# Kernel optimization log

Measured on AMD Instinct MI355X. Metric: run time of the kernel, lower is better.

## Reference

```python
import jax, jax.numpy as jnp
import numpy as np

DIM = 256
NH = 8
HD = DIM // NH
SCALE = HD ** -0.5


def setup_inputs() -> dict:
    key = jax.random.key(0)
    ks = jax.random.split(key, 11)
    Bn, Mh, Mw, C = 2048, 8, 8, DIM
    x = jax.random.normal(ks[0], (Bn, Mh, Mw, C), dtype=jnp.float32)
    y = jax.random.normal(ks[1], (Bn, Mh, Mw, C), dtype=jnp.float32)
    z = jax.random.normal(ks[2], (Bn, Mh, Mw, C), dtype=jnp.float32)
    s = 0.02
    q_w = jax.random.normal(ks[3], (C, C), dtype=jnp.float32) * s
    q_b = jnp.zeros((C,), dtype=jnp.float32)
    k_w = jax.random.normal(ks[4], (C, C), dtype=jnp.float32) * s
    k_b = jnp.zeros((C,), dtype=jnp.float32)
    v_w = jax.random.normal(ks[5], (C, C), dtype=jnp.float32) * s
    v_b = jnp.zeros((C,), dtype=jnp.float32)
    proj_w = jax.random.normal(ks[6], (C, C), dtype=jnp.float32) * s
    proj_b = jnp.zeros((C,), dtype=jnp.float32)
    return {"x": x, "y": y, "z": z, "q_w": q_w, "q_b": q_b, "k_w": k_w,
            "k_b": k_b, "v_w": v_w, "v_b": v_b, "proj_w": proj_w, "proj_b": proj_b}


def softmax_plus_one(a):
    m = jnp.max(a, axis=-1, keepdims=True)
    e = jnp.exp(a - m)
    return e / (jnp.sum(e, axis=-1, keepdims=True) + 1.0)


def reference(x, y, z, q_w, q_b, k_w, k_b, v_w, v_b, proj_w, proj_b):
    Bn, Mh, Mw, C = x.shape
    L = Mh * Mw
    xf = x.reshape(Bn, L, C)
    yf = y.reshape(Bn, L, C)
    # z is rearranged but unused in the original forward

    def heads(t, w, b):
        # torch Linear: t @ w.T + b, then split heads -> (Bn, Nh, L, HD)
        p = t @ w.T + b
        return p.reshape(Bn, L, NH, HD).transpose(0, 2, 1, 3)

    q1 = heads(yf, q_w, q_b) * SCALE
    k1 = heads(xf, k_w, k_b)
    v1 = heads(xf, v_w, v_b)

    attn = jnp.einsum('bnqd,bnkd->bnqk', q1, k1)  # (Bn, Nh, L, L)
    attn = softmax_plus_one(attn)
    y1 = jnp.einsum('bnqk,bnkd->bnqd', attn, v1)  # (Bn, Nh, L, HD)
    y1 = y1.transpose(0, 2, 1, 3).reshape(Bn, Mh, Mw, C)

    out = y + y1
    out = out @ proj_w.T + proj_b
    return out
```

## Files before the change

### kernel.cpp

```cpp
#include <hip/hip_runtime.h>

typedef __bf16 bf16x8 __attribute__((ext_vector_type(8)));
typedef __bf16 bf16x4 __attribute__((ext_vector_type(4)));
typedef short  s16x4  __attribute__((ext_vector_type(4)));
typedef float  f32x4  __attribute__((ext_vector_type(4)));
typedef unsigned int u32x4 __attribute__((ext_vector_type(4)));
typedef unsigned int u32x2 __attribute__((ext_vector_type(2)));
typedef unsigned int u32;
typedef unsigned short u16;

#define DEVI static __device__ __forceinline__

static constexpr float KSCALE = 0.17677669529663687f;

DEVI u32 pk2(float a, float b){
  u16 ha = __builtin_bit_cast(u16, (__bf16)a);
  u16 hb = __builtin_bit_cast(u16, (__bf16)b);
  return (u32)ha | ((u32)hb << 16);
}
DEVI float bfl(u32 bits16){
  union { u32 i; float f; } v; v.i = bits16 << 16; return v.f;
}
DEVI u32x2 pkfrag(f32x4 v){ u32x2 o; o[0]=pk2(v[0],v[1]); o[1]=pk2(v[2],v[3]); return o; }
DEVI bf16x8 ld16(const void* p){ return __builtin_bit_cast(bf16x8, *(const u32x4*)p); }
DEVI f32x4 mfma16(bf16x8 a, bf16x8 b, f32x4 c){
  return __builtin_amdgcn_mfma_f32_16x16x32_bf16(a, b, c, 0, 0, 0);
}
DEVI f32x4 mfma1616(u32x2 a, u32x2 b, f32x4 c){
#if __has_builtin(__builtin_amdgcn_mfma_f32_16x16x16_bf16)
  return __builtin_amdgcn_mfma_f32_16x16x16_bf16(
      __builtin_bit_cast(bf16x4, a), __builtin_bit_cast(bf16x4, b), c, 0, 0, 0);
#elif __has_builtin(__builtin_amdgcn_mfma_f32_16x16x16bf16_1k)
  return __builtin_amdgcn_mfma_f32_16x16x16bf16_1k(
      __builtin_bit_cast(s16x4, a), __builtin_bit_cast(s16x4, b), c, 0, 0, 0);
#else
  asm("v_mfma_f32_16x16x16_bf16 %0, %1, %2, %0" : "+v"(c) : "v"(a), "v"(b));
  return c;
#endif
}

template<bool BW>
DEVI bf16x8 loadw(const u16* wbp, const float* wfp){
  if constexpr (BW){
    return ld16(wbp);
  } else {
    f32x4 a = *(const f32x4*)wfp;
    f32x4 b = *(const f32x4*)(wfp + 4);
    u32x4 pc; pc[0]=pk2(a[0],a[1]); pc[1]=pk2(a[2],a[3]); pc[2]=pk2(b[0],b[1]); pc[3]=pk2(b[2],b[3]);
    return __builtin_bit_cast(bf16x8, pc);
  }
}

__global__ void prep_w(const float* __restrict__ qw, const float* __restrict__ kw,
                       const float* __restrict__ vw, const float* __restrict__ pw,
                       u16* __restrict__ dst){
  int blk = blockIdx.x;
  int l   = threadIdx.x;
  int M = blk >> 7, R = (blk >> 3) & 15, kk = blk & 7;
  const float* W = (M==0) ? qw : (M==1) ? kw : (M==2) ? vw : pw;
  const float* src = W + (R*16 + (l&15))*256 + kk*32 + (l>>4)*8;
  f32x4 a  = *(const f32x4*)src;
  f32x4 b2 = *(const f32x4*)(src + 4);
  u32x4 pc; pc[0]=pk2(a[0],a[1]); pc[1]=pk2(a[2],a[3]); pc[2]=pk2(b2[0],b2[1]); pc[3]=pk2(b2[2],b2[3]);
  *(u32x4*)(dst + (size_t)blk*512 + l*8) = pc;
}

DEVI const u16* wfrag(const u16* wb, int M, int R, int kk, int l){
  return wb + ((((M<<4) + R)<<3) + kk)*512 + l*8;
}

template<bool BW>
__global__ __launch_bounds__(256, 2)
void fused_ca(const float* __restrict__ x, const float* __restrict__ y,
              const u16* __restrict__ wb,
              const float* __restrict__ qwf, const float* __restrict__ kwf,
              const float* __restrict__ vwf, const float* __restrict__ pwf,
              const float* __restrict__ qb, const float* __restrict__ kb,
              const float* __restrict__ vb, const float* __restrict__ pb,
              float* __restrict__ out)
{
  extern __shared__ char smem[];
  const int b  = blockIdx.x;
  const int t  = threadIdx.x;
  const int w  = t >> 6;
  const int l  = t & 63;
  const int lo = l & 15;
  const int g  = l >> 4;
  const u32 swr = (u32)(lo & 7) << 4;

  char* r1 = smem;
  char* Xs = smem + 32768;

  const float* yb = y + (size_t)b * 16384;
  const float* xb = x + (size_t)b * 16384;

  #pragma unroll
  for (int j = 0; j < 16; ++j){
    int idx = t + 256*j;
    int row = idx >> 6;
    int c0  = (idx & 63) * 4;
    f32x4 v = *(const f32x4*)(yb + row*256 + c0);
    u32x2 o; o[0] = pk2(v[0], v[1]); o[1] = pk2(v[2], v[3]);
    *(u32x2*)(r1 + row*512 + ((u32)(c0*2) ^ ((u32)(row&7) << 4))) = o;
  }
  f32x4 xr[8];
  #pragma unroll
  for (int j = 0; j < 8; ++j){
    int idx = t + 256*j;
    xr[j] = *(const f32x4*)(xb + (idx>>6)*256 + (idx & 63)*4);
  }
  __syncthreads();

  u32x2 aqpk[2][8];
  #pragma unroll
  for (int hl = 0; hl < 2; ++hl){
    const int cb = w*64 + hl*32;
    const int Rb = w*4 + hl*2;
    f32x4 aq[2][4] = {};
    #pragma unroll
    for (int kk = 0; kk < 8; ++kk){
      bf16x8 A[2], Bf[4];
      #pragma unroll
      for (int m = 0; m < 2; ++m){
        int off = (cb + 16*m + lo)*256 + kk*32 + 8*g;
        A[m] = loadw<BW>(wfrag(wb, 0, Rb + m, kk, l), qwf + off);
      }
      #pragma unroll
      for (int n = 0; n < 4; ++n)
        Bf[n] = ld16(r1 + (16*n+lo)*512 + ((u32)(kk*64 + 16*g) ^ swr));
      #pragma unroll
      for (int m = 0; m < 2; ++m)
        #pragma unroll
        for (int n = 0; n < 4; ++n)
          aq[m][n] = mfma16(A[m], Bf[n], aq[m][n]);
    }
    #pragma unroll
    for (int m = 0; m < 2; ++m){
      f32x4 bias = *(const f32x4*)(qb + cb + 16*m + 4*g);
      #pragma unroll
      for (int n = 0; n < 4; ++n){
        f32x4 v; 
        #pragma unroll
        for (int r = 0; r < 4; ++r) v[r] = (aq[m][n][r] + bias[r]) * KSCALE;
        aqpk[hl][m*4+n] = pkfrag(v);
      }
    }
    if (hl == 0){
      #pragma unroll
      for (int j = 0; j < 8; ++j){
        int idx = t + 256*j;
        int row = idx >> 6;
        int c0  = (idx & 63) * 4;
        u32x2 o; o[0] = pk2(xr[j][0], xr[j][1]); o[1] = pk2(xr[j][2], xr[j][3]);
        *(u32x2*)(Xs + row*512 + ((u32)(c0*2) ^ ((u32)(row&7) << 4))) = o;
      }
      #pragma unroll
      for (int j = 0; j < 8; ++j){
        int idx = t + 256*(j+8);
        xr[j] = *(const f32x4*)(xb + (idx>>6)*256 + (idx & 63)*4);
      }
    }
  }
  #pragma unroll
  for (int j = 0; j < 8; ++j){
    int idx = t + 256*(j+8);
    int row = idx >> 6;
    int c0  = (idx & 63) * 4;
    u32x2 o; o[0] = pk2(xr[j][0], xr[j][1]); o[1] = pk2(xr[j][2], xr[j][3]);
    *(u32x2*)(Xs + row*512 + ((u32)(c0*2) ^ ((u32)(row&7) << 4))) = o;
  }
  __syncthreads();

  #pragma unroll
  for (int hl = 0; hl < 2; ++hl){
    const int cb = w*64 + hl*32;
    const int Rb = w*4 + hl*2;

    f32x4 ak[2][4] = {};
    f32x4 av[4][2] = {};
    #pragma unroll
    for (int kk = 0; kk < 8; ++kk){
      bf16x8 WA[2], WB2[2], XF[4];
      #pragma unroll
      for (int m = 0; m < 2; ++m){
        int off = (cb + 16*m + lo)*256 + kk*32 + 8*g;
        WA[m] = loadw<BW>(wfrag(wb, 1, Rb + m, kk, l), kwf + off);
      }
      #pragma unroll
      for (int n = 0; n < 2; ++n){
        int off = (cb + 16*n + lo)*256 + kk*32 + 8*g;
        WB2[n] = loadw<BW>(wfrag(wb, 2, Rb + n, kk, l), vwf + off);
      }
      #pragma unroll
      for (int f = 0; f < 4; ++f)
        XF[f] = ld16(Xs + (16*f+lo)*512 + ((u32)(kk*64 + 16*g) ^ swr));
      #pragma unroll
      for (int f = 0; f < 4; ++f){
        #pragma unroll
        for (int m = 0; m < 2; ++m)
          ak[m][f] = mfma16(WA[m], XF[f], ak[m][f]);
        #pragma unroll
        for (int n = 0; n < 2; ++n)
          av[f][n] = mfma16(XF[f], WB2[n], av[f][n]);
      }
    }
    u32x2 akpk[8], avpk[8];
    #pragma unroll
    for (int m = 0; m < 2; ++m){
      f32x4 bias = *(const f32x4*)(kb + cb + 16*m + 4*g);
      #pragma unroll
      for (int f = 0; f < 4; ++f){
        f32x4 v;
        #pragma unroll
        for (int r = 0; r < 4; ++r) v[r] = ak[m][f][r] + bias[r];
        akpk[m*4+f] = pkfrag(v);
      }
    }
    #pragma unroll
    for (int n = 0; n < 2; ++n){
      float bias = vb[cb + 16*n + lo];
      #pragma unroll
      for (int f = 0; f < 4; ++f){
        f32x4 v;
        #pragma unroll
        for (int r = 0; r < 4; ++r) v[r] = av[f][n][r] + bias;
        avpk[f*2+n] = pkfrag(v);
      }
    }

    f32x4 y1h[2][4] = {};
    #pragma unroll
    for (int n = 0; n < 4; ++n){
      f32x4 s4[4];
      #pragma unroll
      for (int f = 0; f < 4; ++f){
        f32x4 acc = {};
        acc = mfma1616(akpk[0*4+f], aqpk[hl][0*4+n], acc);
        acc = mfma1616(akpk[1*4+f], aqpk[hl][1*4+n], acc);
        s4[f] = acc;
      }
      float mx = s4[0][0];
      #pragma unroll
      for (int f = 0; f < 4; ++f)
        #pragma unroll
        for (int r = 0; r < 4; ++r)
          mx = fmaxf(mx, s4[f][r]);
      mx = fmaxf(mx, __shfl_xor(mx, 16));
      mx = fmaxf(mx, __shfl_xor(mx, 32));
      float sum = 0.f;
      #pragma unroll
      for (int f = 0; f < 4; ++f)
        #pragma unroll
        for (int r = 0; r < 4; ++r){
          float e = __expf(s4[f][r] - mx);
          s4[f][r] = e; sum += e;
        }
      sum += __shfl_xor(sum, 16);
      sum += __shfl_xor(sum, 32);
      float rin = 1.0f / (sum + 1.0f);
      u32x2 spk[4];
      #pragma unroll
      for (int f = 0; f < 4; ++f){
        f32x4 v;
        #pragma unroll
        for (int r = 0; r < 4; ++r) v[r] = s4[f][r] * rin;
        spk[f] = pkfrag(v);
      }
      #pragma unroll
      for (int md = 0; md < 2; ++md)
        #pragma unroll
        for (int f = 0; f < 4; ++f)
          y1h[md][n] = mfma1616(avpk[f*2+md], spk[f], y1h[md][n]);
    }

    #pragma unroll
    for (int md = 0; md < 2; ++md)
      #pragma unroll
      for (int n = 0; n < 4; ++n){
        int c0 = cb + 16*md + 4*g;
        char* p = r1 + (16*n+lo)*512 + ((u32)(c0*2) ^ swr);
        u32x2 old = *(const u32x2*)p;
        f32x4 a = y1h[md][n];
        float o0 = bfl(old[0] & 0xffffu) + a[0];
        float o1 = bfl(old[0] >> 16)     + a[1];
        float o2 = bfl(old[1] & 0xffffu) + a[2];
        float o3 = bfl(old[1] >> 16)     + a[3];
        u32x2 nw; nw[0] = pk2(o0, o1); nw[1] = pk2(o2, o3);
        *(u32x2*)p = nw;
      }
  }

  __syncthreads();

  f32x4 ap[4][4] = {};
  #pragma unroll
  for (int kk = 0; kk < 8; ++kk){
    bf16x8 Af[4], Bp[4];
    #pragma unroll
    for (int m = 0; m < 4; ++m)
      Af[m] = ld16(r1 + (16*m+lo)*512 + ((u32)(kk*64 + 16*g) ^ swr));
    #pragma unroll
    for (int n = 0; n < 4; ++n){
      int off = (w*64 + 16*n + lo)*256 + kk*32 + 8*g;
      Bp[n] = loadw<BW>(wfrag(wb, 3, w*4 + n, kk, l), pwf + off);
    }
    #pragma unroll
    for (int m = 0; m < 4; ++m)
      #pragma unroll
      for (int n = 0; n < 4; ++n)
        ap[m][n] = mfma16(Af[m], Bp[n], ap[m][n]);
  }

  float pbv[4];
  #pragma unroll
  for (int n = 0; n < 4; ++n) pbv[n] = pb[w*64 + 16*n + lo];
  #pragma unroll
  for (int m = 0; m < 4; ++m)
    #pragma unroll
    for (int n = 0; n < 4; ++n)
      #pragma unroll
      for (int r = 0; r < 4; ++r)
        ap[m][n][r] += pbv[n];

  float* ob = out + (size_t)b * 16384;
  #pragma unroll
  for (int half = 0; half < 2; ++half){
    __syncthreads();
    #pragma unroll
    for (int mm = 0; mm < 2; ++mm)
      #pragma unroll
      for (int n = 0; n < 4; ++n){
        int col = w*64 + 16*n + lo;
        #pragma unroll
        for (int r = 0; r < 4; ++r){
          int row = mm*16 + 4*g + r;
          u32 byteoff = ((u32)(row*1024 + col*4)) ^ ((u32)(row & 4) << 4);
          *(float*)(r1 + byteoff) = ap[half*2 + mm][n][r];
        }
      }
    __syncthreads();
    #pragma unroll
    for (int i = 0; i < 8; ++i){
      int id  = i*256 + t;
      int row = id >> 6;
      int cc  = id & 63;
      u32 byteoff = (u32)(row*1024) + ((u32)(cc ^ (row & 4)) << 4);
      f32x4 v = *(const f32x4*)(r1 + byteoff);
      *(f32x4*)(ob + (half*32 + row)*256 + cc*4) = v;
    }
  }
}

extern "C" void kernel_launch(void* const* d_in, const int* in_sizes, int n_in,
                              void* d_out, int out_size, void* d_ws, size_t ws_size,
                              hipStream_t stream) {
  (void)n_in; (void)out_size;
  const float* x  = (const float*)d_in[0];
  const float* y  = (const float*)d_in[1];
  const float* qw = (const float*)d_in[3];
  const float* qb = (const float*)d_in[4];
  const float* kw = (const float*)d_in[5];
  const float* kb = (const float*)d_in[6];
  const float* vw = (const float*)d_in[7];
  const float* vb = (const float*)d_in[8];
  const float* pw = (const float*)d_in[9];
  const float* pb = (const float*)d_in[10];
  float* out = (float*)d_out;
  const int Bn = in_sizes[0] / 16384;

  const bool useWs = ws_size >= (size_t)524288;
  if (useWs){
    u16* wsb = (u16*)d_ws;
    prep_w<<<512, 64, 0, stream>>>(qw, kw, vw, pw, wsb);
    (void)hipFuncSetAttribute(reinterpret_cast<const void*>(&fused_ca<true>),
                              hipFuncAttributeMaxDynamicSharedMemorySize, 65536);
    fused_ca<true><<<Bn, 256, 65536, stream>>>(x, y, wsb, qw, kw, vw, pw,
                                               qb, kb, vb, pb, out);
  } else {
    (void)hipFuncSetAttribute(reinterpret_cast<const void*>(&fused_ca<false>),
                              hipFuncAttributeMaxDynamicSharedMemorySize, 65536);
    fused_ca<false><<<Bn, 256, 65536, stream>>>(x, y, (const u16*)d_ws, qw, kw, vw, pw,
                                                qb, kb, vb, pb, out);
  }
}
```

Baseline: 173.0 us.

## Halve shared memory to one 32KB tile and split projection into two GEMMs

```diff
diff --git a/kernel.cpp b/kernel.cpp
--- a/kernel.cpp
+++ b/kernel.cpp
@@ -17,9 +17,6 @@
   u16 ha = __builtin_bit_cast(u16, (__bf16)a);
   u16 hb = __builtin_bit_cast(u16, (__bf16)b);
   return (u32)ha | ((u32)hb << 16);
-}
-DEVI float bfl(u32 bits16){
-  union { u32 i; float f; } v; v.i = bits16 << 16; return v.f;
 }
 DEVI u32x2 pkfrag(f32x4 v){ u32x2 o; o[0]=pk2(v[0],v[1]); o[1]=pk2(v[2],v[3]); return o; }
 DEVI bf16x8 ld16(const void* p){ return __builtin_bit_cast(bf16x8, *(const u32x4*)p); }
@@ -69,8 +66,16 @@
   return wb + ((((M<<4) + R)<<3) + kk)*512 + l*8;
 }
 
+DEVI void stw(char* T, int t, int j, f32x4 v){
+  int idx = t + 256*j;
+  int row = idx >> 6;
+  int c0  = (idx & 63) * 4;
+  u32x2 o; o[0] = pk2(v[0], v[1]); o[1] = pk2(v[2], v[3]);
+  *(u32x2*)(T + row*512 + ((u32)(c0*2) ^ ((u32)(row&7) << 4))) = o;
+}
+
 template<bool BW>
-__global__ __launch_bounds__(256, 2)
+__global__ __launch_bounds__(256, 3)
 void fused_ca(const float* __restrict__ x, const float* __restrict__ y,
               const u16* __restrict__ wb,
               const float* __restrict__ qwf, const float* __restrict__ kwf,
@@ -80,6 +85,7 @@
               float* __restrict__ out)
 {
   extern __shared__ char smem[];
+  char* T = smem;
   const int b  = blockIdx.x;
   const int t  = threadIdx.x;
   const int w  = t >> 6;
@@ -88,30 +94,36 @@
   const int g  = l >> 4;
   const u32 swr = (u32)(lo & 7) << 4;
 
-  char* r1 = smem;
-  char* Xs = smem + 32768;
-
   const float* yb = y + (size_t)b * 16384;
   const float* xb = x + (size_t)b * 16384;
 
-  #pragma unroll
-  for (int j = 0; j < 16; ++j){
-    int idx = t + 256*j;
-    int row = idx >> 6;
-    int c0  = (idx & 63) * 4;
-    f32x4 v = *(const f32x4*)(yb + row*256 + c0);
-    u32x2 o; o[0] = pk2(v[0], v[1]); o[1] = pk2(v[2], v[3]);
-    *(u32x2*)(r1 + row*512 + ((u32)(c0*2) ^ ((u32)(row&7) << 4))) = o;
+  {
+    f32x4 yr[8], yr2[8];
+    #pragma unroll
+    for (int j = 0; j < 8; ++j){
+      int idx = t + 256*j;
+      yr[j] = *(const f32x4*)(yb + (idx>>6)*256 + (idx&63)*4);
+    }
+    #pragma unroll
+    for (int j = 0; j < 8; ++j){
+      int idx = t + 256*(j+8);
+      yr2[j] = *(const f32x4*)(yb + (idx>>6)*256 + (idx&63)*4);
+    }
+    #pragma unroll
+    for (int j = 0; j < 8; ++j) stw(T, t, j, yr[j]);
+    #pragma unroll
+    for (int j = 0; j < 8; ++j) stw(T, t, j+8, yr2[j]);
   }
   f32x4 xr[8];
   #pragma unroll
   for (int j = 0; j < 8; ++j){
     int idx = t + 256*j;
-    xr[j] = *(const f32x4*)(xb + (idx>>6)*256 + (idx & 63)*4);
+    xr[j] = *(const f32x4*)(xb + (idx>>6)*256 + (idx&63)*4);
   }
   __syncthreads();
 
   u32x2 aqpk[2][8];
+  f32x4 xr2[8];
   #pragma unroll
   for (int hl = 0; hl < 2; ++hl){
     const int cb = w*64 + hl*32;
@@ -127,7 +139,7 @@
       }
       #pragma unroll
       for (int n = 0; n < 4; ++n)
-        Bf[n] = ld16(r1 + (16*n+lo)*512 + ((u32)(kk*64 + 16*g) ^ swr));
+        Bf[n] = ld16(T + (16*n+lo)*512 + ((u32)(kk*64 + 16*g) ^ swr));
       #pragma unroll
       for (int m = 0; m < 2; ++m)
         #pragma unroll
@@ -139,7 +151,7 @@
       f32x4 bias = *(const f32x4*)(qb + cb + 16*m + 4*g);
       #pragma unroll
       for (int n = 0; n < 4; ++n){
-        f32x4 v; 
+        f32x4 v;
         #pragma unroll
         for (int r = 0; r < 4; ++r) v[r] = (aq[m][n][r] + bias[r]) * KSCALE;
         aqpk[hl][m*4+n] = pkfrag(v);
@@ -148,34 +160,24 @@
     if (hl == 0){
       #pragma unroll
       for (int j = 0; j < 8; ++j){
-        int idx = t + 256*j;
-        int row = idx >> 6;
-        int c0  = (idx & 63) * 4;
-        u32x2 o; o[0] = pk2(xr[j][0], xr[j][1]); o[1] = pk2(xr[j][2], xr[j][3]);
-        *(u32x2*)(Xs + row*512 + ((u32)(c0*2) ^ ((u32)(row&7) << 4))) = o;
-      }
-      #pragma unroll
-      for (int j = 0; j < 8; ++j){
         int idx = t + 256*(j+8);
-        xr[j] = *(const f32x4*)(xb + (idx>>6)*256 + (idx & 63)*4);
-      }
-    }
-  }
-  #pragma unroll
-  for (int j = 0; j < 8; ++j){
-    int idx = t + 256*(j+8);
-    int row = idx >> 6;
-    int c0  = (idx & 63) * 4;
-    u32x2 o; o[0] = pk2(xr[j][0], xr[j][1]); o[1] = pk2(xr[j][2], xr[j][3]);
-    *(u32x2*)(Xs + row*512 + ((u32)(c0*2) ^ ((u32)(row&7) << 4))) = o;
-  }
-  __syncthreads();
-
+        xr2[j] = *(const f32x4*)(xb + (idx>>6)*256 + (idx&63)*4);
+      }
+    }
+  }
+  __syncthreads();
+
+  #pragma unroll
+  for (int j = 0; j < 8; ++j) stw(T, t, j, xr[j]);
+  #pragma unroll
+  for (int j = 0; j < 8; ++j) stw(T, t, j+8, xr2[j]);
+  __syncthreads();
+
+  u32x2 akpk[2][8], avpk[2][8];
   #pragma unroll
   for (int hl = 0; hl < 2; ++hl){
     const int cb = w*64 + hl*32;
     const int Rb = w*4 + hl*2;
-
     f32x4 ak[2][4] = {};
     f32x4 av[4][2] = {};
     #pragma unroll
@@ -193,7 +195,7 @@
       }
       #pragma unroll
       for (int f = 0; f < 4; ++f)
-        XF[f] = ld16(Xs + (16*f+lo)*512 + ((u32)(kk*64 + 16*g) ^ swr));
+        XF[f] = ld16(T + (16*f+lo)*512 + ((u32)(kk*64 + 16*g) ^ swr));
       #pragma unroll
       for (int f = 0; f < 4; ++f){
         #pragma unroll
@@ -204,7 +206,6 @@
           av[f][n] = mfma16(XF[f], WB2[n], av[f][n]);
       }
     }
-    u32x2 akpk[8], avpk[8];
     #pragma unroll
     for (int m = 0; m < 2; ++m){
       f32x4 bias = *(const f32x4*)(kb + cb + 16*m + 4*g);
@@ -213,7 +214,7 @@
         f32x4 v;
         #pragma unroll
         for (int r = 0; r < 4; ++r) v[r] = ak[m][f][r] + bias[r];
-        akpk[m*4+f] = pkfrag(v);
+        akpk[hl][m*4+f] = pkfrag(v);
       }
     }
     #pragma unroll
@@ -224,10 +225,15 @@
         f32x4 v;
         #pragma unroll
         for (int r = 0; r < 4; ++r) v[r] = av[f][n][r] + bias;
-        avpk[f*2+n] = pkfrag(v);
-      }
-    }
-
+        avpk[hl][f*2+n] = pkfrag(v);
+      }
+    }
+  }
+  __syncthreads();
+
+  #pragma unroll
+  for (int hl = 0; hl < 2; ++hl){
+    const int cb = w*64 + hl*32;
     f32x4 y1h[2][4] = {};
     #pragma unroll
     for (int n = 0; n < 4; ++n){
@@ -235,8 +241,8 @@
       #pragma unroll
       for (int f = 0; f < 4; ++f){
         f32x4 acc = {};
-        acc = mfma1616(akpk[0*4+f], aqpk[hl][0*4+n], acc);
-        acc = mfma1616(akpk[1*4+f], aqpk[hl][1*4+n], acc);
+        acc = mfma1616(akpk[hl][0*4+f], aqpk[hl][0*4+n], acc);
+        acc = mfma1616(akpk[hl][1*4+f], aqpk[hl][1*4+n], acc);
         s4[f] = acc;
       }
       float mx = s4[0][0];
@@ -270,35 +276,31 @@
       for (int md = 0; md < 2; ++md)
         #pragma unroll
         for (int f = 0; f < 4; ++f)
-          y1h[md][n] = mfma1616(avpk[f*2+md], spk[f], y1h[md][n]);
-    }
-
+          y1h[md][n] = mfma1616(avpk[hl][f*2+md], spk[f], y1h[md][n]);
+    }
     #pragma unroll
     for (int md = 0; md < 2; ++md)
       #pragma unroll
       for (int n = 0; n < 4; ++n){
         int c0 = cb + 16*md + 4*g;
-        char* p = r1 + (16*n+lo)*512 + ((u32)(c0*2) ^ swr);
-        u32x2 old = *(const u32x2*)p;
-        f32x4 a = y1h[md][n];
-        float o0 = bfl(old[0] & 0xffffu) + a[0];
-        float o1 = bfl(old[0] >> 16)     + a[1];
-        float o2 = bfl(old[1] & 0xffffu) + a[2];
-        float o3 = bfl(old[1] >> 16)     + a[3];
-        u32x2 nw; nw[0] = pk2(o0, o1); nw[1] = pk2(o2, o3);
-        *(u32x2*)p = nw;
-      }
-  }
-
+        *(u32x2*)(T + (16*n+lo)*512 + ((u32)(c0*2) ^ swr)) = pkfrag(y1h[md][n]);
+      }
+  }
   __syncthreads();
 
   f32x4 ap[4][4] = {};
+  f32x4 yra[8];
+  #pragma unroll
+  for (int j = 0; j < 8; ++j){
+    int idx = t + 256*j;
+    yra[j] = *(const f32x4*)(yb + (idx>>6)*256 + (idx&63)*4);
+  }
   #pragma unroll
   for (int kk = 0; kk < 8; ++kk){
     bf16x8 Af[4], Bp[4];
     #pragma unroll
     for (int m = 0; m < 4; ++m)
-      Af[m] = ld16(r1 + (16*m+lo)*512 + ((u32)(kk*64 + 16*g) ^ swr));
+      Af[m] = ld16(T + (16*m+lo)*512 + ((u32)(kk*64 + 16*g) ^ swr));
     #pragma unroll
     for (int n = 0; n < 4; ++n){
       int off = (w*64 + 16*n + lo)*256 + kk*32 + 8*g;
@@ -310,6 +312,37 @@
       for (int n = 0; n < 4; ++n)
         ap[m][n] = mfma16(Af[m], Bp[n], ap[m][n]);
   }
+  f32x4 yrb[8];
+  #pragma unroll
+  for (int j = 0; j < 8; ++j){
+    int idx = t + 256*(j+8);
+    yrb[j] = *(const f32x4*)(yb + (idx>>6)*256 + (idx&63)*4);
+  }
+  __syncthreads();
+
+  #pragma unroll
+  for (int j = 0; j < 8; ++j) stw(T, t, j, yra[j]);
+  #pragma unroll
+  for (int j = 0; j < 8; ++j) stw(T, t, j+8, yrb[j]);
+  __syncthreads();
+
+  #pragma unroll
+  for (int kk = 0; kk < 8; ++kk){
+    bf16x8 Af[4], Bp[4];
+    #pragma unroll
+    for (int m = 0; m < 4; ++m)
+      Af[m] = ld16(T + (16*m+lo)*512 + ((u32)(kk*64 + 16*g) ^ swr));
+    #pragma unroll
+    for (int n = 0; n < 4; ++n){
+      int off = (w*64 + 16*n + lo)*256 + kk*32 + 8*g;
+      Bp[n] = loadw<BW>(wfrag(wb, 3, w*4 + n, kk, l), pwf + off);
+    }
+    #pragma unroll
+    for (int m = 0; m < 4; ++m)
+      #pragma unroll
+      for (int n = 0; n < 4; ++n)
+        ap[m][n] = mfma16(Af[m], Bp[n], ap[m][n]);
+  }
 
   float pbv[4];
   #pragma unroll
@@ -335,7 +368,7 @@
         for (int r = 0; r < 4; ++r){
           int row = mm*16 + 4*g + r;
           u32 byteoff = ((u32)(row*1024 + col*4)) ^ ((u32)(row & 4) << 4);
-          *(float*)(r1 + byteoff) = ap[half*2 + mm][n][r];
+          *(float*)(T + byteoff) = ap[half*2 + mm][n][r];
         }
       }
     __syncthreads();
@@ -345,7 +378,7 @@
       int row = id >> 6;
       int cc  = id & 63;
       u32 byteoff = (u32)(row*1024) + ((u32)(cc ^ (row & 4)) << 4);
-      f32x4 v = *(const f32x4*)(r1 + byteoff);
+      f32x4 v = *(const f32x4*)(T + byteoff);
       *(f32x4*)(ob + (half*32 + row)*256 + cc*4) = v;
     }
   }
@@ -372,14 +405,10 @@
   if (useWs){
     u16* wsb = (u16*)d_ws;
     prep_w<<<512, 64, 0, stream>>>(qw, kw, vw, pw, wsb);
-    (void)hipFuncSetAttribute(reinterpret_cast<const void*>(&fused_ca<true>),
-                              hipFuncAttributeMaxDynamicSharedMemorySize, 65536);
-    fused_ca<true><<<Bn, 256, 65536, stream>>>(x, y, wsb, qw, kw, vw, pw,
+    fused_ca<true><<<Bn, 256, 32768, stream>>>(x, y, wsb, qw, kw, vw, pw,
                                                qb, kb, vb, pb, out);
   } else {
-    (void)hipFuncSetAttribute(reinterpret_cast<const void*>(&fused_ca<false>),
-                              hipFuncAttributeMaxDynamicSharedMemorySize, 65536);
-    fused_ca<false><<<Bn, 256, 65536, stream>>>(x, y, (const u16*)d_ws, qw, kw, vw, pw,
+    fused_ca<false><<<Bn, 256, 32768, stream>>>(x, y, (const u16*)d_ws, qw, kw, vw, pw,
                                                 qb, kb, vb, pb, out);
   }
 }
```

Measured after the change: 425.2 us. 2.46x slower.

## Drop X shared-memory staging, load X fragments from global to raise occupancy

Applied to the files above, without the earlier changes.

```diff
diff --git a/kernel.cpp b/kernel.cpp
--- a/kernel.cpp
+++ b/kernel.cpp
@@ -70,7 +70,7 @@
 }
 
 template<bool BW>
-__global__ __launch_bounds__(256, 2)
+__global__ __launch_bounds__(256, 3)
 void fused_ca(const float* __restrict__ x, const float* __restrict__ y,
               const u16* __restrict__ wb,
               const float* __restrict__ qwf, const float* __restrict__ kwf,
@@ -80,6 +80,7 @@
               float* __restrict__ out)
 {
   extern __shared__ char smem[];
+  char* r1 = smem;
   const int b  = blockIdx.x;
   const int t  = threadIdx.x;
   const int w  = t >> 6;
@@ -88,9 +89,6 @@
   const int g  = l >> 4;
   const u32 swr = (u32)(lo & 7) << 4;
 
-  char* r1 = smem;
-  char* Xs = smem + 32768;
-
   const float* yb = y + (size_t)b * 16384;
   const float* xb = x + (size_t)b * 16384;
 
@@ -103,12 +101,6 @@
     u32x2 o; o[0] = pk2(v[0], v[1]); o[1] = pk2(v[2], v[3]);
     *(u32x2*)(r1 + row*512 + ((u32)(c0*2) ^ ((u32)(row&7) << 4))) = o;
   }
-  f32x4 xr[8];
-  #pragma unroll
-  for (int j = 0; j < 8; ++j){
-    int idx = t + 256*j;
-    xr[j] = *(const f32x4*)(xb + (idx>>6)*256 + (idx & 63)*4);
-  }
   __syncthreads();
 
   u32x2 aqpk[2][8];
@@ -139,35 +131,12 @@
       f32x4 bias = *(const f32x4*)(qb + cb + 16*m + 4*g);
       #pragma unroll
       for (int n = 0; n < 4; ++n){
-        f32x4 v; 
+        f32x4 v;
         #pragma unroll
         for (int r = 0; r < 4; ++r) v[r] = (aq[m][n][r] + bias[r]) * KSCALE;
         aqpk[hl][m*4+n] = pkfrag(v);
       }
     }
-    if (hl == 0){
-      #pragma unroll
-      for (int j = 0; j < 8; ++j){
-        int idx = t + 256*j;
-        int row = idx >> 6;
-        int c0  = (idx & 63) * 4;
-        u32x2 o; o[0] = pk2(xr[j][0], xr[j][1]); o[1] = pk2(xr[j][2], xr[j][3]);
-        *(u32x2*)(Xs + row*512 + ((u32)(c0*2) ^ ((u32)(row&7) << 4))) = o;
-      }
-      #pragma unroll
-      for (int j = 0; j < 8; ++j){
-        int idx = t + 256*(j+8);
-        xr[j] = *(const f32x4*)(xb + (idx>>6)*256 + (idx & 63)*4);
-      }
-    }
-  }
-  #pragma unroll
-  for (int j = 0; j < 8; ++j){
-    int idx = t + 256*(j+8);
-    int row = idx >> 6;
-    int c0  = (idx & 63) * 4;
-    u32x2 o; o[0] = pk2(xr[j][0], xr[j][1]); o[1] = pk2(xr[j][2], xr[j][3]);
-    *(u32x2*)(Xs + row*512 + ((u32)(c0*2) ^ ((u32)(row&7) << 4))) = o;
   }
   __syncthreads();
 
@@ -192,8 +161,14 @@
         WB2[n] = loadw<BW>(wfrag(wb, 2, Rb + n, kk, l), vwf + off);
       }
       #pragma unroll
-      for (int f = 0; f < 4; ++f)
-        XF[f] = ld16(Xs + (16*f+lo)*512 + ((u32)(kk*64 + 16*g) ^ swr));
+      for (int f = 0; f < 4; ++f){
+        const float* px = xb + (16*f + lo)*256 + kk*32 + 8*g;
+        f32x4 u0 = *(const f32x4*)px;
+        f32x4 u1 = *(const f32x4*)(px + 4);
+        u32x4 pc; pc[0]=pk2(u0[0],u0[1]); pc[1]=pk2(u0[2],u0[3]);
+                  pc[2]=pk2(u1[0],u1[1]); pc[3]=pk2(u1[2],u1[3]);
+        XF[f] = __builtin_bit_cast(bf16x8, pc);
+      }
       #pragma unroll
       for (int f = 0; f < 4; ++f){
         #pragma unroll
@@ -372,14 +347,10 @@
   if (useWs){
     u16* wsb = (u16*)d_ws;
     prep_w<<<512, 64, 0, stream>>>(qw, kw, vw, pw, wsb);
-    (void)hipFuncSetAttribute(reinterpret_cast<const void*>(&fused_ca<true>),
-                              hipFuncAttributeMaxDynamicSharedMemorySize, 65536);
-    fused_ca<true><<<Bn, 256, 65536, stream>>>(x, y, wsb, qw, kw, vw, pw,
+    fused_ca<true><<<Bn, 256, 32768, stream>>>(x, y, wsb, qw, kw, vw, pw,
                                                qb, kb, vb, pb, out);
   } else {
-    (void)hipFuncSetAttribute(reinterpret_cast<const void*>(&fused_ca<false>),
-                              hipFuncAttributeMaxDynamicSharedMemorySize, 65536);
-    fused_ca<false><<<Bn, 256, 65536, stream>>>(x, y, (const u16*)d_ws, qw, kw, vw, pw,
+    fused_ca<false><<<Bn, 256, 32768, stream>>>(x, y, (const u16*)d_ws, qw, kw, vw, pw,
                                                 qb, kb, vb, pb, out);
   }
 }
```

Result: slower. 410.9 us (+137.5%).

## Split work across eight waves per block, one head per wave

Applied to the files above, without the earlier changes.

```diff
diff --git a/kernel.cpp b/kernel.cpp
--- a/kernel.cpp
+++ b/kernel.cpp
@@ -69,8 +69,15 @@
   return wb + ((((M<<4) + R)<<3) + kk)*512 + l*8;
 }
 
+DEVI void stw(char* T, int idx, f32x4 v){
+  int row = idx >> 6;
+  int c0  = (idx & 63) * 4;
+  u32x2 o; o[0] = pk2(v[0], v[1]); o[1] = pk2(v[2], v[3]);
+  *(u32x2*)(T + row*512 + ((u32)(c0*2) ^ ((u32)(row&7) << 4))) = o;
+}
+
 template<bool BW>
-__global__ __launch_bounds__(256, 2)
+__global__ __launch_bounds__(512, 4)
 void fused_ca(const float* __restrict__ x, const float* __restrict__ y,
               const u16* __restrict__ wb,
               const float* __restrict__ qwf, const float* __restrict__ kwf,
@@ -80,6 +87,8 @@
               float* __restrict__ out)
 {
   extern __shared__ char smem[];
+  char* r1 = smem;
+  char* Xs = smem + 32768;
   const int b  = blockIdx.x;
   const int t  = threadIdx.x;
   const int w  = t >> 6;
@@ -87,35 +96,33 @@
   const int lo = l & 15;
   const int g  = l >> 4;
   const u32 swr = (u32)(lo & 7) << 4;
-
-  char* r1 = smem;
-  char* Xs = smem + 32768;
+  const int cb = w*32;
+  const int Rb = w*2;
 
   const float* yb = y + (size_t)b * 16384;
   const float* xb = x + (size_t)b * 16384;
 
-  #pragma unroll
-  for (int j = 0; j < 16; ++j){
-    int idx = t + 256*j;
-    int row = idx >> 6;
-    int c0  = (idx & 63) * 4;
-    f32x4 v = *(const f32x4*)(yb + row*256 + c0);
-    u32x2 o; o[0] = pk2(v[0], v[1]); o[1] = pk2(v[2], v[3]);
-    *(u32x2*)(r1 + row*512 + ((u32)(c0*2) ^ ((u32)(row&7) << 4))) = o;
-  }
-  f32x4 xr[8];
-  #pragma unroll
-  for (int j = 0; j < 8; ++j){
-    int idx = t + 256*j;
-    xr[j] = *(const f32x4*)(xb + (idx>>6)*256 + (idx & 63)*4);
-  }
-  __syncthreads();
-
-  u32x2 aqpk[2][8];
-  #pragma unroll
-  for (int hl = 0; hl < 2; ++hl){
-    const int cb = w*64 + hl*32;
-    const int Rb = w*4 + hl*2;
+  {
+    f32x4 yr[8], xr[8];
+    #pragma unroll
+    for (int j = 0; j < 8; ++j){
+      int idx = t + 512*j;
+      yr[j] = *(const f32x4*)(yb + (idx>>6)*256 + (idx&63)*4);
+    }
+    #pragma unroll
+    for (int j = 0; j < 8; ++j){
+      int idx = t + 512*j;
+      xr[j] = *(const f32x4*)(xb + (idx>>6)*256 + (idx&63)*4);
+    }
+    #pragma unroll
+    for (int j = 0; j < 8; ++j) stw(r1, t + 512*j, yr[j]);
+    #pragma unroll
+    for (int j = 0; j < 8; ++j) stw(Xs, t + 512*j, xr[j]);
+  }
+  __syncthreads();
+
+  u32x2 aqpk[8];
+  {
     f32x4 aq[2][4] = {};
     #pragma unroll
     for (int kk = 0; kk < 8; ++kk){
@@ -139,54 +146,53 @@
       f32x4 bias = *(const f32x4*)(qb + cb + 16*m + 4*g);
       #pragma unroll
       for (int n = 0; n < 4; ++n){
-        f32x4 v; 
+        f32x4 v;
         #pragma unroll
         for (int r = 0; r < 4; ++r) v[r] = (aq[m][n][r] + bias[r]) * KSCALE;
-        aqpk[hl][m*4+n] = pkfrag(v);
-      }
-    }
-    if (hl == 0){
-      #pragma unroll
-      for (int j = 0; j < 8; ++j){
-        int idx = t + 256*j;
-        int row = idx >> 6;
-        int c0  = (idx & 63) * 4;
-        u32x2 o; o[0] = pk2(xr[j][0], xr[j][1]); o[1] = pk2(xr[j][2], xr[j][3]);
-        *(u32x2*)(Xs + row*512 + ((u32)(c0*2) ^ ((u32)(row&7) << 4))) = o;
-      }
-      #pragma unroll
-      for (int j = 0; j < 8; ++j){
-        int idx = t + 256*(j+8);
-        xr[j] = *(const f32x4*)(xb + (idx>>6)*256 + (idx & 63)*4);
-      }
-    }
-  }
-  #pragma unroll
-  for (int j = 0; j < 8; ++j){
-    int idx = t + 256*(j+8);
-    int row = idx >> 6;
-    int c0  = (idx & 63) * 4;
-    u32x2 o; o[0] = pk2(xr[j][0], xr[j][1]); o[1] = pk2(xr[j][2], xr[j][3]);
-    *(u32x2*)(Xs + row*512 + ((u32)(c0*2) ^ ((u32)(row&7) << 4))) = o;
-  }
-  __syncthreads();
-
-  #pragma unroll
-  for (int hl = 0; hl < 2; ++hl){
-    const int cb = w*64 + hl*32;
-    const int Rb = w*4 + hl*2;
-
+        aqpk[m*4+n] = pkfrag(v);
+      }
+    }
+  }
+
+  u32x2 akpk[8];
+  {
     f32x4 ak[2][4] = {};
-    f32x4 av[4][2] = {};
     #pragma unroll
     for (int kk = 0; kk < 8; ++kk){
-      bf16x8 WA[2], WB2[2], XF[4];
+      bf16x8 WA[2], XF[4];
       #pragma unroll
       for (int m = 0; m < 2; ++m){
         int off = (cb + 16*m + lo)*256 + kk*32 + 8*g;
         WA[m] = loadw<BW>(wfrag(wb, 1, Rb + m, kk, l), kwf + off);
       }
       #pragma unroll
+      for (int f = 0; f < 4; ++f)
+        XF[f] = ld16(Xs + (16*f+lo)*512 + ((u32)(kk*64 + 16*g) ^ swr));
+      #pragma unroll
+      for (int f = 0; f < 4; ++f)
+        #pragma unroll
+        for (int m = 0; m < 2; ++m)
+          ak[m][f] = mfma16(WA[m], XF[f], ak[m][f]);
+    }
+    #pragma unroll
+    for (int m = 0; m < 2; ++m){
+      f32x4 bias = *(const f32x4*)(kb + cb + 16*m + 4*g);
+      #pragma unroll
+      for (int f = 0; f < 4; ++f){
+        f32x4 v;
+        #pragma unroll
+        for (int r = 0; r < 4; ++r) v[r] = ak[m][f][r] + bias[r];
+        akpk[m*4+f] = pkfrag(v);
+      }
+    }
+  }
+  u32x2 avpk[8];
+  {
+    f32x4 av[4][2] = {};
+    #pragma unroll
+    for (int kk = 0; kk < 8; ++kk){
+      bf16x8 WB2[2], XF[4];
+      #pragma unroll
       for (int n = 0; n < 2; ++n){
         int off = (cb + 16*n + lo)*256 + kk*32 + 8*g;
         WB2[n] = loadw<BW>(wfrag(wb, 2, Rb + n, kk, l), vwf + off);
@@ -195,39 +201,26 @@
       for (int f = 0; f < 4; ++f)
         XF[f] = ld16(Xs + (16*f+lo)*512 + ((u32)(kk*64 + 16*g) ^ swr));
       #pragma unroll
-      for (int f = 0; f < 4; ++f){
-        #pragma unroll
-        for (int m = 0; m < 2; ++m)
-          ak[m][f] = mfma16(WA[m], XF[f], ak[m][f]);
+      for (int f = 0; f < 4; ++f)
         #pragma unroll
         for (int n = 0; n < 2; ++n)
           av[f][n] = mfma16(XF[f], WB2[n], av[f][n]);
-      }
-    }
-    u32x2 akpk[8], avpk[8];
-    #pragma unroll
-    for (int m = 0; m < 2; ++m){
-      f32x4 bias = *(const f32x4*)(kb + cb + 16*m + 4*g);
+    }
+    #pragma unroll
+    for (int n = 0; n < 2; ++n){
+      float bias = vb[cb + 16*n + lo];
       #pragma unroll
       for (int f = 0; f < 4; ++f){
         f32x4 v;
         #pragma unroll
-        for (int r = 0; r < 4; ++r) v[r] = ak[m][f][r] + bias[r];
-        akpk[m*4+f] = pkfrag(v);
-      }
-    }
-    #pragma unroll
-    for (int n = 0; n < 2; ++n){
-      float bias = vb[cb + 16*n + lo];
-      #pragma unroll
-      for (int f = 0; f < 4; ++f){
-        f32x4 v;
-        #pragma unroll
         for (int r = 0; r < 4; ++r) v[r] = av[f][n][r] + bias;
         avpk[f*2+n] = pkfrag(v);
       }
     }
-
+  }
+  __syncthreads();
+
+  {
     f32x4 y1h[2][4] = {};
     #pragma unroll
     for (int n = 0; n < 4; ++n){
@@ -235,8 +228,8 @@
       #pragma unroll
       for (int f = 0; f < 4; ++f){
         f32x4 acc = {};
-        acc = mfma1616(akpk[0*4+f], aqpk[hl][0*4+n], acc);
-        acc = mfma1616(akpk[1*4+f], aqpk[hl][1*4+n], acc);
+        acc = mfma1616(akpk[0*4+f], aqpk[0*4+n], acc);
+        acc = mfma1616(akpk[1*4+f], aqpk[1*4+n], acc);
         s4[f] = acc;
       }
       float mx = s4[0][0];
@@ -289,65 +282,62 @@
         *(u32x2*)p = nw;
       }
   }
-
-  __syncthreads();
-
-  f32x4 ap[4][4] = {};
+  __syncthreads();
+
+  f32x4 ap[4][2] = {};
   #pragma unroll
   for (int kk = 0; kk < 8; ++kk){
-    bf16x8 Af[4], Bp[4];
+    bf16x8 Af[4], Bp[2];
     #pragma unroll
     for (int m = 0; m < 4; ++m)
       Af[m] = ld16(r1 + (16*m+lo)*512 + ((u32)(kk*64 + 16*g) ^ swr));
     #pragma unroll
-    for (int n = 0; n < 4; ++n){
-      int off = (w*64 + 16*n + lo)*256 + kk*32 + 8*g;
-      Bp[n] = loadw<BW>(wfrag(wb, 3, w*4 + n, kk, l), pwf + off);
+    for (int n = 0; n < 2; ++n){
+      int off = (cb + 16*n + lo)*256 + kk*32 + 8*g;
+      Bp[n] = loadw<BW>(wfrag(wb, 3, Rb + n, kk, l), pwf + off);
     }
     #pragma unroll
     for (int m = 0; m < 4; ++m)
       #pragma unroll
-      for (int n = 0; n < 4; ++n)
+      for (int n = 0; n < 2; ++n)
         ap[m][n] = mfma16(Af[m], Bp[n], ap[m][n]);
   }
-
-  float pbv[4];
-  #pragma unroll
-  for (int n = 0; n < 4; ++n) pbv[n] = pb[w*64 + 16*n + lo];
+  {
+    float pbv[2];
+    #pragma unroll
+    for (int n = 0; n < 2; ++n) pbv[n] = pb[cb + 16*n + lo];
+    #pragma unroll
+    for (int m = 0; m < 4; ++m)
+      #pragma unroll
+      for (int n = 0; n < 2; ++n)
+        #pragma unroll
+        for (int r = 0; r < 4; ++r)
+          ap[m][n][r] += pbv[n];
+  }
+
+  float* ob = out + (size_t)b * 16384;
+  __syncthreads();
   #pragma unroll
   for (int m = 0; m < 4; ++m)
     #pragma unroll
-    for (int n = 0; n < 4; ++n)
-      #pragma unroll
-      for (int r = 0; r < 4; ++r)
-        ap[m][n][r] += pbv[n];
-
-  float* ob = out + (size_t)b * 16384;
+    for (int n = 0; n < 2; ++n){
+      int col = cb + 16*n + lo;
+      #pragma unroll
+      for (int r = 0; r < 4; ++r){
+        int row = 16*m + 4*g + r;
+        u32 byteoff = ((u32)(row*1024 + col*4)) ^ ((u32)(row & 4) << 4);
+        *(float*)(smem + byteoff) = ap[m][n][r];
+      }
+    }
+  __syncthreads();
   #pragma unroll
-  for (int half = 0; half < 2; ++half){
-    __syncthreads();
-    #pragma unroll
-    for (int mm = 0; mm < 2; ++mm)
-      #pragma unroll
-      for (int n = 0; n < 4; ++n){
-        int col = w*64 + 16*n + lo;
-        #pragma unroll
-        for (int r = 0; r < 4; ++r){
-          int row = mm*16 + 4*g + r;
-          u32 byteoff = ((u32)(row*1024 + col*4)) ^ ((u32)(row & 4) << 4);
-          *(float*)(r1 + byteoff) = ap[half*2 + mm][n][r];
-        }
-      }
-    __syncthreads();
-    #pragma unroll
-    for (int i = 0; i < 8; ++i){
-      int id  = i*256 + t;
-      int row = id >> 6;
-      int cc  = id & 63;
-      u32 byteoff = (u32)(row*1024) + ((u32)(cc ^ (row & 4)) << 4);
-      f32x4 v = *(const f32x4*)(r1 + byteoff);
-      *(f32x4*)(ob + (half*32 + row)*256 + cc*4) = v;
-    }
+  for (int i = 0; i < 8; ++i){
+    int id  = i*512 + t;
+    int row = id >> 6;
+    int cc  = id & 63;
+    u32 byteoff = (u32)(row*1024) + ((u32)(cc ^ (row & 4)) << 4);
+    f32x4 v = *(const f32x4*)(smem + byteoff);
+    *(f32x4*)(ob + row*256 + cc*4) = v;
   }
 }
 
@@ -374,12 +364,12 @@
     prep_w<<<512, 64, 0, stream>>>(qw, kw, vw, pw, wsb);
     (void)hipFuncSetAttribute(reinterpret_cast<const void*>(&fused_ca<true>),
                               hipFuncAttributeMaxDynamicSharedMemorySize, 65536);
-    fused_ca<true><<<Bn, 256, 65536, stream>>>(x, y, wsb, qw, kw, vw, pw,
+    fused_ca<true><<<Bn, 512, 65536, stream>>>(x, y, wsb, qw, kw, vw, pw,
                                                qb, kb, vb, pb, out);
   } else {
     (void)hipFuncSetAttribute(reinterpret_cast<const void*>(&fused_ca<false>),
                               hipFuncAttributeMaxDynamicSharedMemorySize, 65536);
-    fused_ca<false><<<Bn, 256, 65536, stream>>>(x, y, (const u16*)d_ws, qw, kw, vw, pw,
+    fused_ca<false><<<Bn, 512, 65536, stream>>>(x, y, (const u16*)d_ws, qw, kw, vw, pw,
                                                 qb, kb, vb, pb, out);
   }
 }
```

Measured after the change: 236.4 us. 1.37x slower.
